# Kernel optimization log

Hardware: AMD Instinct MI355X
Metric: run time of the kernel (lower is better)

## Reference

```python
import jax, jax.numpy as jnp
import numpy as np

B, T, C, L = 1024, 256, 100, 64  # batch, time steps, classes (blank=C-1), label length
NEG = -1e30   # safe -inf for log-space DP
EPS = 1e-7    # Keras K.epsilon() added before log


def setup_inputs() -> dict:
    key = jax.random.key(0)
    k1, k2 = jax.random.split(key)
    logits = jax.random.normal(k1, (B, T, C), dtype=jnp.float32)
    y_pred = jax.nn.softmax(logits, axis=-1)  # ctc_batch_cost expects probabilities
    y_true = jax.random.randint(k2, (B, L), 0, C - 1)  # labels in [0, C-2]; blank=C-1
    return {"y_true": y_true, "y_pred": y_pred}


def ctc_loss(y_true, y_pred):
    """Faithful K.ctc_batch_cost with full input/label lengths, blank = C-1."""
    Bb, Tt, Cc = y_pred.shape
    Ll = y_true.shape[1]
    S = 2 * Ll + 1  # extended label lattice: blank-interleaved
    blank = Cc - 1

    # extended labels: [blank, l0, blank, l1, ..., blank]
    ext = jnp.full((Bb, S), blank, dtype=y_true.dtype).at[:, 1::2].set(y_true)
    # skip-transition allowed when ext[s] is non-blank and differs from ext[s-2]
    ext_m2 = jnp.concatenate([jnp.full((Bb, 2), -1, ext.dtype), ext[:, :-2]], axis=1)
    allow = (ext != blank) & (ext != ext_m2)  # [B,S]

    logp = jnp.log(y_pred + EPS)  # [B,T,C]
    # gather log-probs on the lattice once: [B,T,S]
    lp_ext = jnp.take_along_axis(
        logp, jnp.broadcast_to(ext[:, None, :], (Bb, Tt, S)), axis=2)
    lp_seq = jnp.moveaxis(lp_ext, 1, 0)  # [T,B,S] for scan

    # alpha init: only states 0 (blank) and 1 (first label) reachable at t=0
    alpha0 = jnp.where(jnp.arange(S)[None, :] < 2, lp_seq[0], NEG)

    def shift(a, k):
        return jnp.concatenate(
            [jnp.full((Bb, k), NEG, a.dtype), a[:, :-k]], axis=1)

    def step(alpha, lp_t):
        new = jnp.logaddexp(
            jnp.logaddexp(alpha, shift(alpha, 1)),
            jnp.where(allow, shift(alpha, 2), NEG)) + lp_t
        return new, None

    alphaT, _ = jax.lax.scan(step, alpha0, lp_seq[1:])
    # total prob = alpha[T-1, S-1] + alpha[T-1, S-2]
    loss = -jnp.logaddexp(alphaT[:, -1], alphaT[:, -2])
    return loss[:, None]  # ctc_batch_cost returns shape [B,1]


def reference(y_true, y_pred):
    return ctc_loss(y_true, y_pred)
```

## Files before the change

kernel.cpp:

```cpp
#include <hip/hip_runtime.h>

#define B_ 1024
#define T_ 256
#define C_ 100
#define L_ 64
#define EPS_ 1e-7f
#define LN2 0.69314718055994530942f

#define CH 8
#define NCH 16
#define DEPTH 4
#define SLOTS 5
#define SLOTF 832
#define BROW (T_ * C_ * 4)

#define LOG2F(x) __builtin_amdgcn_logf(x)

typedef const __attribute__((address_space(1))) void GV;
typedef __attribute__((address_space(3))) void LV;

__device__ __forceinline__ void gload_lds16(const void* g, void* l) {
    __builtin_amdgcn_global_load_lds((GV*)g, (LV*)l, 16, 0, 0);
}
__device__ __forceinline__ void gload_lds4(const void* g, void* l) {
    __builtin_amdgcn_global_load_lds((GV*)g, (LV*)l, 4, 0, 0);
}

__device__ __forceinline__ float dpp_shr1(float x) {
    return __int_as_float(__builtin_amdgcn_update_dpp(
        0, __float_as_int(x), 0x138, 0xf, 0xf, false));
}
__device__ __forceinline__ float dpp_shl1(float x) {
    return __int_as_float(__builtin_amdgcn_update_dpp(
        0, __float_as_int(x), 0x130, 0xf, 0xf, false));
}

#define PLAN(x0_, x1_, x2_) do {                                          \
    float m_ = fmaxf(fmaxf(x0_, x1_), x2_);                               \
    _Pragma("unroll")                                                     \
    for (int d_ = 1; d_ < 64; d_ <<= 1) m_ = fmaxf(m_, __shfl_xor(m_, d_)); \
    const int e_ = (__float_as_int(m_) >> 23) & 255;                      \
    rs_K = 127 - e_;                                                      \
    rs_scale = __int_as_float((254 - e_) << 23);           \
} while (0)

#define APPLY(x0_, x1_, x2_) do { x0_ *= rs_scale; x1_ *= rs_scale;       \
    x2_ *= rs_scale; Sacc += rs_K; } while (0)

#define FSTEP(pb_, pl_) do {                                              \
    const float up1 = dpp_shr1(a1);                                       \
    const float s   = allow ? up1 : 0.0f;                                 \
    const float n0  = (a0 + up1) * (pb_);                                 \
    const float n1  = ((a1 + a0) + s) * (pl_);                            \
    const float n2  = (a2 + a1) * (pb_);                                  \
    a0 = n0; a1 = n1; a2 = n2;                                            \
} while (0)

#define BSTEP(pb_, pl_) do {                                              \
    const float db0 = dpp_shl1(a0);                                       \
    const float db1 = dpp_shl1(a1);                                       \
    const float sc0 = is63 ? a2 : db0;                                    \
    const float sk  = allowN ? db1 : 0.0f;                                \
    const float n0  = (a0 + a1) * (pb_);                                  \
    const float n1  = ((a1 + sc0) + sk) * (pl_);                          \
    const float n2  = a2 * (pb_);                                         \
    a0 = n0; a1 = n1; a2 = n2;                                            \
} while (0)

#define WAITC(c_) do {                                                    \
    if ((c_) <= NCH - 1 - 3)  asm volatile("s_waitcnt vmcnt(12)" ::: "memory"); \
    else if ((c_) == NCH - 3) asm volatile("s_waitcnt vmcnt(8)"  ::: "memory"); \
    else if ((c_) == NCH - 2) asm volatile("s_waitcnt vmcnt(4)"  ::: "memory"); \
    else                      asm volatile("s_waitcnt vmcnt(0)"  ::: "memory"); \
} while (0)

#define SISSUE(wv_, c_, off0_) do {                                       \
    float* __restrict__ slot_ = &ring[wv_][(c_) % SLOTS][0];              \
    _Pragma("unroll")                                                     \
    for (int k_ = 0; k_ < 3; ++k_)                                        \
        gload_lds16(bb + ((unsigned)(off0_) + k_ * 1024u + ((unsigned)lane << 4)), \
                    slot_ + k_ * 256);                                    \
    {                                                                     \
        unsigned o_ = (unsigned)(off0_) + 3072u + ((unsigned)lane << 2);  \
        o_ = o_ < (BROW - 4u) ? o_ : (BROW - 4u);                         \
        gload_lds4(bb + o_, slot_ + 768);                                 \
    }                                                                     \
} while (0)

__global__ __launch_bounds__(128) void ctc_kernel(
    const int* __restrict__ y_true,
    const float* __restrict__ y_pred,
    float* __restrict__ out)
{
    __shared__ float ring[2][SLOTS][SLOTF];
    __shared__ float sG0[64], sG1[64];
    __shared__ float sG2;
    __shared__ int   sSaccB;

    const int tid  = threadIdx.x;
    const int lane = tid & 63;
    const int wv   = tid >> 6;
    const int b    = blockIdx.x;

    const float* __restrict__ base = y_pred + (size_t)b * T_ * C_;
    const char*  __restrict__ bb   = (const char*)base;
    const int  label   = y_true[b * L_ + lane];
    const int  labprev = __shfl_up(label, 1);
    const bool allow   = (lane == 0) || (label != labprev);
    const bool is63    = (lane == 63);
    const bool allowN  = (bool)__shfl_down((int)allow, 1);

    float a0 = 0.0f, a1 = 0.0f, a2 = 0.0f;
    float rs_scale = 1.0f;
    int   rs_K = 0, Sacc = 0;

    if (wv == 0) {
        #pragma unroll
        for (int c = 0; c < DEPTH; ++c) SISSUE(0, c, c * 3200);

        #pragma unroll
        for (int c = 0; c < NCH; ++c) {
            WAITC(c);
            if (c + DEPTH < NCH) SISSUE(0, c + DEPTH, (c + DEPTH) * 3200);
            const float* __restrict__ sl = ring[0][c % SLOTS];
            if (c == 0) {
                a0 = (lane == 0) ? (sl[99] + EPS_) : 0.0f;
                a1 = (lane == 0) ? (sl[label] + EPS_) : 0.0f;
                a2 = 0.0f;
                PLAN(a0, a1, a2);
                #pragma unroll
                for (int j = 1; j < CH; ++j)
                    FSTEP(sl[j * 100 + 99] + EPS_, sl[j * 100 + label] + EPS_);
            } else {
                APPLY(a0, a1, a2);
                PLAN(a0, a1, a2);
                #pragma unroll
                for (int j = 0; j < CH; ++j)
                    FSTEP(sl[j * 100 + 99] + EPS_, sl[j * 100 + label] + EPS_);
            }
        }

        APPLY(a0, a1, a2);
        PLAN(a0, a1, a2);
        APPLY(a0, a1, a2);
    } else {
        #pragma unroll
        for (int c = 0; c < DEPTH; ++c) SISSUE(1, c, 99200 - c * 3200);

        #pragma unroll
        for (int c = 0; c < NCH; ++c) {
            WAITC(c);
            if (c + DEPTH < NCH) SISSUE(1, c + DEPTH, 99200 - (c + DEPTH) * 3200);
            const float* __restrict__ sl = ring[1][c % SLOTS];
            if (c == 0) {
                a2 = sl[799] + EPS_;
                a1 = is63 ? (sl[700 + label] + EPS_) : 0.0f;
                a0 = 0.0f;
                PLAN(a0, a1, a2);
                #pragma unroll
                for (int j = 1; j < CH; ++j)
                    BSTEP(sl[(7 - j) * 100 + 99] + EPS_, sl[(7 - j) * 100 + label] + EPS_);
            } else {
                APPLY(a0, a1, a2);
                PLAN(a0, a1, a2);
                #pragma unroll
                for (int j = 0; j < CH; ++j)
                    BSTEP(sl[(7 - j) * 100 + 99] + EPS_, sl[(7 - j) * 100 + label] + EPS_);
            }
        }

        APPLY(a0, a1, a2);
        PLAN(a0, a1, a2);
        APPLY(a0, a1, a2);

        const float db0 = dpp_shl1(a0);
        const float db1 = dpp_shl1(a1);
        sG0[lane] = a0 + a1;
        sG1[lane] = a1 + (is63 ? a2 : db0) + (allowN ? db1 : 0.0f);
        if (is63) { sG2 = a2; sSaccB = Sacc; }
    }

    __syncthreads();

    if (wv == 0) {
        float prod = a0 * sG0[lane] + a1 * sG1[lane];
        if (is63) prod += a2 * sG2;
        #pragma unroll
        for (int d = 1; d < 64; d <<= 1) prod += __shfl_xor(prod, d);
        if (lane == 0)
            out[b] = -LN2 * (LOG2F(prod) - (float)(Sacc + sSaccB));
    }
}

extern "C" void kernel_launch(void* const* d_in, const int* in_sizes, int n_in,
                              void* d_out, int out_size, void* d_ws, size_t ws_size,
                              hipStream_t stream) {
    const int*   y_true = (const int*)d_in[0];
    const float* y_pred = (const float*)d_in[1];
    float*       out    = (float*)d_out;

    ctc_kernel<<<dim3(B_), dim3(128), 0, stream>>>(y_true, y_pred, out);
}
```

Measured before the change: 24.36 us.

## Split loading into dedicated producer waves with barrier-synchronized chunk handoff

Adds two producer waves per block that issue the global-to-LDS loads for the forward and backward directions. The two compute waves now only run the recurrence. The handoff uses a __syncthreads per chunk, and the producers issue s_waitcnt before each barrier. This aims to remove load-issue and wait latency from the serial compute critical path. In exchange it doubles block size, which can lower occupancy, and adds 16 block-wide barriers that couple the forward and backward waves' progress.

```diff
diff --git a/kernel.cpp b/kernel.cpp
--- a/kernel.cpp
+++ b/kernel.cpp
@@ -9,7 +9,6 @@
 
 #define CH 8
 #define NCH 16
-#define DEPTH 4
 #define SLOTS 5
 #define SLOTF 832
 #define BROW (T_ * C_ * 4)
@@ -25,6 +24,8 @@
 __device__ __forceinline__ void gload_lds4(const void* g, void* l) {
     __builtin_amdgcn_global_load_lds((GV*)g, (LV*)l, 4, 0, 0);
 }
+
+#define WV(n_) asm volatile("s_waitcnt vmcnt(" #n_ ")" ::: "memory")
 
 __device__ __forceinline__ float dpp_shr1(float x) {
     return __int_as_float(__builtin_amdgcn_update_dpp(
@@ -67,15 +68,8 @@
     a0 = n0; a1 = n1; a2 = n2;                                            \
 } while (0)
 
-#define WAITC(c_) do {                                                    \
-    if ((c_) <= NCH - 1 - 3)  asm volatile("s_waitcnt vmcnt(12)" ::: "memory"); \
-    else if ((c_) == NCH - 3) asm volatile("s_waitcnt vmcnt(8)"  ::: "memory"); \
-    else if ((c_) == NCH - 2) asm volatile("s_waitcnt vmcnt(4)"  ::: "memory"); \
-    else                      asm volatile("s_waitcnt vmcnt(0)"  ::: "memory"); \
-} while (0)
-
-#define SISSUE(wv_, c_, off0_) do {                                       \
-    float* __restrict__ slot_ = &ring[wv_][(c_) % SLOTS][0];              \
+#define SISSUE(dir_, sidx_, off0_) do {                                   \
+    float* __restrict__ slot_ = &ring[dir_][sidx_][0];                    \
     _Pragma("unroll")                                                     \
     for (int k_ = 0; k_ < 3; ++k_)                                        \
         gload_lds16(bb + ((unsigned)(off0_) + k_ * 1024u + ((unsigned)lane << 4)), \
@@ -87,7 +81,21 @@
     }                                                                     \
 } while (0)
 
-__global__ __launch_bounds__(128) void ctc_kernel(
+#define FBODY(sl_) do {                                                   \
+    APPLY(a0, a1, a2); PLAN(a0, a1, a2);                                  \
+    _Pragma("unroll")                                                     \
+    for (int j = 0; j < CH; ++j)                                          \
+        FSTEP((sl_)[j * 100 + 99] + EPS_, (sl_)[j * 100 + label] + EPS_); \
+} while (0)
+
+#define BBODY(sl_) do {                                                   \
+    APPLY(a0, a1, a2); PLAN(a0, a1, a2);                                  \
+    _Pragma("unroll")                                                     \
+    for (int j = 0; j < CH; ++j)                                          \
+        BSTEP((sl_)[(7 - j) * 100 + 99] + EPS_, (sl_)[(7 - j) * 100 + label] + EPS_); \
+} while (0)
+
+__global__ __launch_bounds__(256) void ctc_kernel(
     const int* __restrict__ y_true,
     const float* __restrict__ y_pred,
     float* __restrict__ out)
@@ -99,7 +107,7 @@
 
     const int tid  = threadIdx.x;
     const int lane = tid & 63;
-    const int wv   = tid >> 6;
+    const int wave = tid >> 6;
     const int b    = blockIdx.x;
 
     const float* __restrict__ base = y_pred + (size_t)b * T_ * C_;
@@ -114,14 +122,22 @@
     float rs_scale = 1.0f;
     int   rs_K = 0, Sacc = 0;
 
-    if (wv == 0) {
+    if (wave >= 2) {
+        const int d_ = wave - 2;
         #pragma unroll
-        for (int c = 0; c < DEPTH; ++c) SISSUE(0, c, c * 3200);
-
-        #pragma unroll
-        for (int c = 0; c < NCH; ++c) {
-            WAITC(c);
-            if (c + DEPTH < NCH) SISSUE(0, c + DEPTH, (c + DEPTH) * 3200);
+        for (int c = 0; c < 4; ++c) {
+            const unsigned off = d_ ? (99200u - (unsigned)c * 3200u)
+                                    : ((unsigned)c * 3200u);
+            SISSUE(d_, c, off);
+        }
+        WV(12);
+    }
+
+    #pragma unroll
+    for (int c = 0; c < NCH; ++c) {
+        __syncthreads();
+
+        if (wave == 0) {
             const float* __restrict__ sl = ring[0][c % SLOTS];
             if (c == 0) {
                 a0 = (lane == 0) ? (sl[99] + EPS_) : 0.0f;
@@ -132,25 +148,9 @@
                 for (int j = 1; j < CH; ++j)
                     FSTEP(sl[j * 100 + 99] + EPS_, sl[j * 100 + label] + EPS_);
             } else {
-                APPLY(a0, a1, a2);
-                PLAN(a0, a1, a2);
-                #pragma unroll
-                for (int j = 0; j < CH; ++j)
-                    FSTEP(sl[j * 100 + 99] + EPS_, sl[j * 100 + label] + EPS_);
+                FBODY(sl);
             }
-        }
-
-        APPLY(a0, a1, a2);
-        PLAN(a0, a1, a2);
-        APPLY(a0, a1, a2);
-    } else {
-        #pragma unroll
-        for (int c = 0; c < DEPTH; ++c) SISSUE(1, c, 99200 - c * 3200);
-
-        #pragma unroll
-        for (int c = 0; c < NCH; ++c) {
-            WAITC(c);
-            if (c + DEPTH < NCH) SISSUE(1, c + DEPTH, 99200 - (c + DEPTH) * 3200);
+        } else if (wave == 1) {
             const float* __restrict__ sl = ring[1][c % SLOTS];
             if (c == 0) {
                 a2 = sl[799] + EPS_;
@@ -161,18 +161,30 @@
                 for (int j = 1; j < CH; ++j)
                     BSTEP(sl[(7 - j) * 100 + 99] + EPS_, sl[(7 - j) * 100 + label] + EPS_);
             } else {
-                APPLY(a0, a1, a2);
-                PLAN(a0, a1, a2);
-                #pragma unroll
-                for (int j = 0; j < CH; ++j)
-                    BSTEP(sl[(7 - j) * 100 + 99] + EPS_, sl[(7 - j) * 100 + label] + EPS_);
+                BBODY(sl);
             }
+        } else {
+            const int d_ = wave - 2;
+            if (c + 4 < NCH) {
+                const unsigned off = d_ ? (99200u - (unsigned)(c + 4) * 3200u)
+                                        : ((unsigned)(c + 4) * 3200u);
+                SISSUE(d_, (c + 4) % SLOTS, off);
+            }
+            if (c <= 11)      { WV(12); }
+            else if (c == 12) { WV(8); }
+            else if (c == 13) { WV(4); }
+            else if (c == 14) { WV(0); }
         }
-
+    }
+
+    if (wave == 0) {
         APPLY(a0, a1, a2);
         PLAN(a0, a1, a2);
         APPLY(a0, a1, a2);
-
+    } else if (wave == 1) {
+        APPLY(a0, a1, a2);
+        PLAN(a0, a1, a2);
+        APPLY(a0, a1, a2);
         const float db0 = dpp_shl1(a0);
         const float db1 = dpp_shl1(a1);
         sG0[lane] = a0 + a1;
@@ -182,7 +194,7 @@
 
     __syncthreads();
 
-    if (wv == 0) {
+    if (wave == 0) {
         float prod = a0 * sG0[lane] + a1 * sG1[lane];
         if (is63) prod += a2 * sG2;
         #pragma unroll
@@ -199,5 +211,5 @@
     const float* y_pred = (const float*)d_in[1];
     float*       out    = (float*)d_out;
 
-    ctc_kernel<<<dim3(B_), dim3(128), 0, stream>>>(y_true, y_pred, out);
-}
+    ctc_kernel<<<dim3(B_), dim3(256), 0, stream>>>(y_true, y_pred, out);
+}
```

Measured after the change: 24.32 us. No clear change (-0.2%).
